# Optimization experiments

Measured on AMD Instinct MI355X. Metric: run time of the kernel, lower is better.

Reference implementation:

```python
import jax, jax.numpy as jnp
import numpy as np

STRIDE = (16, 16)
PADDING = (0, 0)


def setup_inputs() -> dict:
    key = jax.random.key(0)
    k1, k2, k3 = jax.random.split(key, 3)
    x = jax.random.normal(k1, (16, 12, 512, 512), dtype=jnp.float32)
    weight = jax.random.normal(k2, (768, 1, 16, 16), dtype=jnp.float32) * 0.02
    bias = jax.random.normal(k3, (768,), dtype=jnp.float32) * 0.02
    return {"x": x, "weight": weight, "bias": bias}


def reference(x, weight, bias):
    # Faithful to the torch module: groups=c conv with the shared filter
    # repeated per input channel, then mean over the channel axis, then bias.
    b, c, h, w = x.shape
    o = weight.shape[0]
    # groups=c conv with repeated weight == independent conv of each channel
    # with the same (o,1,kh,kw) filter; fold channels into batch.
    xc = x.reshape(b * c, 1, h, w)
    y = jax.lax.conv_general_dilated(
        xc, weight,
        window_strides=STRIDE,
        padding=[(PADDING[0], PADDING[0]), (PADDING[1], PADDING[1])],
        dimension_numbers=("NCHW", "OIHW", "NCHW"),
    )  # (b*c, o, H', W')
    hp, wp = y.shape[-2], y.shape[-1]
    y = y.reshape(b, c, o, hp, wp).mean(axis=1)  # (b, o, H', W')
    y = y + bias[None, :, None, None]
    return y
```

## Files before the change

### kernel.cpp

```cpp
#include <hip/hip_runtime.h>
#include <hip/hip_bf16.h>

#define BATCH 16
#define CIN   12
#define HIMG  512
#define WIMG  512
#define OCH   768
#define KDIM  256
#define HW    (HIMG*WIMG)
#define NPATCH 1024

typedef __attribute__((ext_vector_type(8))) short short8;
typedef __attribute__((ext_vector_type(4))) float f32x4;

__global__ void wpack_kernel(const float* __restrict__ w, short8* __restrict__ wbp) {
    int u = blockIdx.x * 256 + threadIdx.x;
    int lane = u & 63;
    int kk   = (u >> 6) & 7;
    int ot   = u >> 9;
    int o = ot * 16 + (lane & 15);
    int k = kk * 32 + (lane >> 4) * 8;
    const float* src = w + (size_t)o * KDIM + k;
    float4 v0 = *reinterpret_cast<const float4*>(src);
    float4 v1 = *reinterpret_cast<const float4*>(src + 4);
    union { short8 s; __hip_bfloat16 h[8]; } t;
    t.h[0] = __float2bfloat16(v0.x);
    t.h[1] = __float2bfloat16(v0.y);
    t.h[2] = __float2bfloat16(v0.z);
    t.h[3] = __float2bfloat16(v0.w);
    t.h[4] = __float2bfloat16(v1.x);
    t.h[5] = __float2bfloat16(v1.y);
    t.h[6] = __float2bfloat16(v1.z);
    t.h[7] = __float2bfloat16(v1.w);
    wbp[u] = t.s;
}

#define LDB 264

__global__ __launch_bounds__(512, 4) void fused_kernel(
        const short8* __restrict__ wbp,
        const float*  __restrict__ x,
        const float*  __restrict__ bias,
        float* __restrict__ out) {
    __shared__ short Bl[32][LDB];

    const int tid = threadIdx.x;
    const int b  = blockIdx.x >> 5;
    const int is = blockIdx.x & 31;

    {
        const int col = (tid & 127) * 4;
        const int r0  = tid >> 7;
        const int j   = col >> 4;
        const int s0  = col & 15;
        const float* xb = x + (size_t)b * CIN * HW + (size_t)(is * 16) * WIMG + col;
        const float inv = 1.0f / 12.0f;
        #pragma unroll
        for (int p = 0; p < 4; ++p) {
            const int r = p * 4 + r0;
            const float* px = xb + (size_t)r * WIMG;
            float sx = 0.f, sy = 0.f, sz = 0.f, sw = 0.f;
            #pragma unroll
            for (int c = 0; c < CIN; ++c) {
                float4 v = *reinterpret_cast<const float4*>(px + (size_t)c * HW);
                sx += v.x; sy += v.y; sz += v.z; sw += v.w;
            }
            union { ushort4 u4; __hip_bfloat16 h[4]; } o;
            o.h[0] = __float2bfloat16(sx * inv);
            o.h[1] = __float2bfloat16(sy * inv);
            o.h[2] = __float2bfloat16(sz * inv);
            o.h[3] = __float2bfloat16(sw * inv);
            *reinterpret_cast<ushort4*>(&Bl[j][r * 16 + s0]) = o.u4;
        }
    }
    __syncthreads();

    const int lane = tid & 63;
    const int wv   = tid >> 6;
    const int lrow = lane & 15;
    const int lg   = lane >> 4;

    f32x4 acc[6][2] = {};
    const short8* wp = wbp + (size_t)(wv * 6) * 8 * 64 + lane;

    #pragma unroll
    for (int kk = 0; kk < 8; ++kk) {
        short8 af[6], bf[2];
        #pragma unroll
        for (int fo = 0; fo < 6; ++fo)
            af[fo] = wp[(size_t)(fo * 8 + kk) * 64];
        #pragma unroll
        for (int fm = 0; fm < 2; ++fm)
            bf[fm] = *reinterpret_cast<const short8*>(&Bl[fm * 16 + lrow][kk * 32 + lg * 8]);
        #pragma unroll
        for (int fo = 0; fo < 6; ++fo)
            #pragma unroll
            for (int fm = 0; fm < 2; ++fm)
                acc[fo][fm] = __builtin_amdgcn_mfma_f32_16x16x32_bf16(af[fo], bf[fm], acc[fo][fm], 0, 0, 0);
    }

    const int p0 = is * 32;
    float* ob = out + (size_t)b * OCH * NPATCH + p0;
    #pragma unroll
    for (int fo = 0; fo < 6; ++fo) {
        const int obase = wv * 96 + fo * 16 + lg * 4;
        #pragma unroll
        for (int r = 0; r < 4; ++r) {
            const int o = obase + r;
            const float bv = bias[o];
            float* orow = ob + (size_t)o * NPATCH;
            #pragma unroll
            for (int fm = 0; fm < 2; ++fm)
                orow[fm * 16 + lrow] = acc[fo][fm][r] + bv;
        }
    }
}

extern "C" void kernel_launch(void* const* d_in, const int* in_sizes, int n_in,
                              void* d_out, int out_size, void* d_ws, size_t ws_size,
                              hipStream_t stream) {
    const float* x    = (const float*)d_in[0];
    const float* w    = (const float*)d_in[1];
    const float* bias = (const float*)d_in[2];
    float* out = (float*)d_out;

    short8* wbp = (short8*)d_ws;

    wpack_kernel<<<96, 256, 0, stream>>>(w, wbp);
    fused_kernel<<<BATCH * 32, 512, 0, stream>>>(wbp, x, bias, out);
}
```

Measured before the change: 53.51 us.

## Software-pipeline channel-mean loads with MFMA chunks using double buffers

Splits the patch-row reduction into four chunks with two register buffers, so the global loads for the next chunk are issued while the MFMAs consume the finished chunk's K range from LDS. Loads become nontemporal, and the occupancy hint in launch_bounds is removed. The goal is to hide the memory latency of the 12-channel x reads behind compute. The cost is 96 extra VGPRs of buffers and the lost occupancy hint, which can reduce waves per CU. The kernel is mostly bandwidth bound, so the overlap may matter less than occupancy.

```diff
diff --git a/kernel.cpp b/kernel.cpp
--- a/kernel.cpp
+++ b/kernel.cpp
@@ -21,8 +21,8 @@
     int o = ot * 16 + (lane & 15);
     int k = kk * 32 + (lane >> 4) * 8;
     const float* src = w + (size_t)o * KDIM + k;
-    float4 v0 = *reinterpret_cast<const float4*>(src);
-    float4 v1 = *reinterpret_cast<const float4*>(src + 4);
+    f32x4 v0 = *reinterpret_cast<const f32x4*>(src);
+    f32x4 v1 = *reinterpret_cast<const f32x4*>(src + 4);
     union { short8 s; __hip_bfloat16 h[8]; } t;
     t.h[0] = __float2bfloat16(v0.x);
     t.h[1] = __float2bfloat16(v0.y);
@@ -37,7 +37,7 @@
 
 #define LDB 264
 
-__global__ __launch_bounds__(512, 4) void fused_kernel(
+__global__ __launch_bounds__(512) void fused_kernel(
         const short8* __restrict__ wbp,
         const float*  __restrict__ x,
         const float*  __restrict__ bias,
@@ -48,56 +48,84 @@
     const int b  = blockIdx.x >> 5;
     const int is = blockIdx.x & 31;
 
-    {
-        const int col = (tid & 127) * 4;
-        const int r0  = tid >> 7;
-        const int j   = col >> 4;
-        const int s0  = col & 15;
-        const float* xb = x + (size_t)b * CIN * HW + (size_t)(is * 16) * WIMG + col;
-        const float inv = 1.0f / 12.0f;
-        #pragma unroll
-        for (int p = 0; p < 4; ++p) {
-            const int r = p * 4 + r0;
-            const float* px = xb + (size_t)r * WIMG;
-            float sx = 0.f, sy = 0.f, sz = 0.f, sw = 0.f;
-            #pragma unroll
-            for (int c = 0; c < CIN; ++c) {
-                float4 v = *reinterpret_cast<const float4*>(px + (size_t)c * HW);
-                sx += v.x; sy += v.y; sz += v.z; sw += v.w;
-            }
-            union { ushort4 u4; __hip_bfloat16 h[4]; } o;
-            o.h[0] = __float2bfloat16(sx * inv);
-            o.h[1] = __float2bfloat16(sy * inv);
-            o.h[2] = __float2bfloat16(sz * inv);
-            o.h[3] = __float2bfloat16(sw * inv);
-            *reinterpret_cast<ushort4*>(&Bl[j][r * 16 + s0]) = o.u4;
-        }
-    }
-    __syncthreads();
+    const int col = (tid & 127) * 4;
+    const int r0  = tid >> 7;
+    const int j   = col >> 4;
+    const int s0  = col & 15;
+    const float* xb = x + (size_t)b * CIN * HW + (size_t)(is * 16) * WIMG + col;
+    const float inv = 1.0f / 12.0f;
 
     const int lane = tid & 63;
     const int wv   = tid >> 6;
     const int lrow = lane & 15;
     const int lg   = lane >> 4;
+    const short8* wp = wbp + (size_t)(wv * 6) * 8 * 64 + lane;
 
     f32x4 acc[6][2] = {};
-    const short8* wp = wbp + (size_t)(wv * 6) * 8 * 64 + lane;
+    f32x4 bufA[CIN], bufB[CIN];
 
-    #pragma unroll
-    for (int kk = 0; kk < 8; ++kk) {
-        short8 af[6], bf[2];
-        #pragma unroll
-        for (int fo = 0; fo < 6; ++fo)
-            af[fo] = wp[(size_t)(fo * 8 + kk) * 64];
-        #pragma unroll
-        for (int fm = 0; fm < 2; ++fm)
-            bf[fm] = *reinterpret_cast<const short8*>(&Bl[fm * 16 + lrow][kk * 32 + lg * 8]);
-        #pragma unroll
-        for (int fo = 0; fo < 6; ++fo)
-            #pragma unroll
-            for (int fm = 0; fm < 2; ++fm)
-                acc[fo][fm] = __builtin_amdgcn_mfma_f32_16x16x32_bf16(af[fo], bf[fm], acc[fo][fm], 0, 0, 0);
+#define ISSUE(buf, ch)                                                         \
+    {                                                                          \
+        const float* p_ = xb + (size_t)((ch) * 4 + r0) * WIMG;                 \
+        _Pragma("unroll")                                                      \
+        for (int c = 0; c < CIN; ++c)                                          \
+            buf[c] = __builtin_nontemporal_load(                               \
+                reinterpret_cast<const f32x4*>(p_ + (size_t)c * HW));          \
     }
+
+#define REDUCE_STORE(buf, ch)                                                  \
+    {                                                                          \
+        float sx = 0.f, sy = 0.f, sz = 0.f, sw = 0.f;                          \
+        _Pragma("unroll")                                                      \
+        for (int c = 0; c < CIN; ++c) {                                        \
+            sx += buf[c].x; sy += buf[c].y; sz += buf[c].z; sw += buf[c].w;    \
+        }                                                                      \
+        union { ushort4 u4; __hip_bfloat16 h[4]; } o_;                         \
+        o_.h[0] = __float2bfloat16(sx * inv);                                  \
+        o_.h[1] = __float2bfloat16(sy * inv);                                  \
+        o_.h[2] = __float2bfloat16(sz * inv);                                  \
+        o_.h[3] = __float2bfloat16(sw * inv);                                  \
+        *reinterpret_cast<ushort4*>(&Bl[j][((ch) * 4 + r0) * 16 + s0]) = o_.u4;\
+    }
+
+#define MFMA_CHUNK(ch)                                                         \
+    {                                                                          \
+        _Pragma("unroll")                                                      \
+        for (int k2 = 0; k2 < 2; ++k2) {                                       \
+            const int kk = (ch) * 2 + k2;                                      \
+            short8 af[6], bf[2];                                               \
+            _Pragma("unroll")                                                  \
+            for (int fo = 0; fo < 6; ++fo)                                     \
+                af[fo] = wp[(size_t)(fo * 8 + kk) * 64];                       \
+            _Pragma("unroll")                                                  \
+            for (int fm = 0; fm < 2; ++fm)                                     \
+                bf[fm] = *reinterpret_cast<const short8*>(                     \
+                    &Bl[fm * 16 + lrow][kk * 32 + lg * 8]);                    \
+            _Pragma("unroll")                                                  \
+            for (int fo = 0; fo < 6; ++fo)                                     \
+                _Pragma("unroll")                                              \
+                for (int fm = 0; fm < 2; ++fm)                                 \
+                    acc[fo][fm] = __builtin_amdgcn_mfma_f32_16x16x32_bf16(     \
+                        af[fo], bf[fm], acc[fo][fm], 0, 0, 0);                 \
+        }                                                                      \
+    }
+
+    ISSUE(bufA, 0);
+    ISSUE(bufB, 1);
+    REDUCE_STORE(bufA, 0);
+    __syncthreads();
+    ISSUE(bufA, 2);
+    MFMA_CHUNK(0);
+    REDUCE_STORE(bufB, 1);
+    __syncthreads();
+    ISSUE(bufB, 3);
+    MFMA_CHUNK(1);
+    REDUCE_STORE(bufA, 2);
+    __syncthreads();
+    MFMA_CHUNK(2);
+    REDUCE_STORE(bufB, 3);
+    __syncthreads();
+    MFMA_CHUNK(3);
 
     const int p0 = is * 32;
     float* ob = out + (size_t)b * OCH * NPATCH + p0;
```

Measured after the change: 59.09 us. 10.4% more time.

## Split channel-mean into a wide standalone kernel merged with weight packing

Applied to the files above, without the earlier changes.

Moves the 12-channel mean reduction out of the 512-block GEMM kernel into a separate 4096-block kernel that writes a bf16 mean image to workspace. The weight-pack work is folded into the same launch as extra blocks. The GEMM kernel now loads the precomputed bf16 tile. The aim is to raise memory-level parallelism for the dominant input read, at the cost of an extra intermediate write and read and a kernel boundary.

```diff
diff --git a/kernel.cpp b/kernel.cpp
--- a/kernel.cpp
+++ b/kernel.cpp
@@ -10,37 +10,63 @@
 #define HW    (HIMG*WIMG)
 #define NPATCH 1024
 
+#define MEAN_BLOCKS 4096
+#define PACK_BLOCKS 96
+
 typedef __attribute__((ext_vector_type(8))) short short8;
 typedef __attribute__((ext_vector_type(4))) float f32x4;
 
-__global__ void wpack_kernel(const float* __restrict__ w, short8* __restrict__ wbp) {
-    int u = blockIdx.x * 256 + threadIdx.x;
-    int lane = u & 63;
-    int kk   = (u >> 6) & 7;
-    int ot   = u >> 9;
-    int o = ot * 16 + (lane & 15);
-    int k = kk * 32 + (lane >> 4) * 8;
-    const float* src = w + (size_t)o * KDIM + k;
-    float4 v0 = *reinterpret_cast<const float4*>(src);
-    float4 v1 = *reinterpret_cast<const float4*>(src + 4);
-    union { short8 s; __hip_bfloat16 h[8]; } t;
-    t.h[0] = __float2bfloat16(v0.x);
-    t.h[1] = __float2bfloat16(v0.y);
-    t.h[2] = __float2bfloat16(v0.z);
-    t.h[3] = __float2bfloat16(v0.w);
-    t.h[4] = __float2bfloat16(v1.x);
-    t.h[5] = __float2bfloat16(v1.y);
-    t.h[6] = __float2bfloat16(v1.z);
-    t.h[7] = __float2bfloat16(v1.w);
-    wbp[u] = t.s;
+__global__ __launch_bounds__(256) void mean_pack_kernel(
+        const float* __restrict__ x, __hip_bfloat16* __restrict__ xm,
+        const float* __restrict__ w, short8* __restrict__ wbp) {
+    const int bid = blockIdx.x;
+    if (bid < MEAN_BLOCKS) {
+        int idx = bid * 256 + threadIdx.x;
+        int b = idx >> 16;
+        int pos = (idx & 65535) << 2;
+        const float* px = x + (size_t)b * CIN * HW + pos;
+        float sx = 0.f, sy = 0.f, sz = 0.f, sw = 0.f;
+        #pragma unroll
+        for (int c = 0; c < CIN; ++c) {
+            f32x4 v = *reinterpret_cast<const f32x4*>(px + (size_t)c * HW);
+            sx += v.x; sy += v.y; sz += v.z; sw += v.w;
+        }
+        const float inv = 1.0f / 12.0f;
+        union { ushort4 u4; __hip_bfloat16 h[4]; } o;
+        o.h[0] = __float2bfloat16(sx * inv);
+        o.h[1] = __float2bfloat16(sy * inv);
+        o.h[2] = __float2bfloat16(sz * inv);
+        o.h[3] = __float2bfloat16(sw * inv);
+        *reinterpret_cast<ushort4*>(xm + (size_t)idx * 4) = o.u4;
+    } else {
+        int u = (bid - MEAN_BLOCKS) * 256 + threadIdx.x;
+        int lane = u & 63;
+        int kk   = (u >> 6) & 7;
+        int ot   = u >> 9;
+        int o = ot * 16 + (lane & 15);
+        int k = kk * 32 + (lane >> 4) * 8;
+        const float* src = w + (size_t)o * KDIM + k;
+        f32x4 v0 = *reinterpret_cast<const f32x4*>(src);
+        f32x4 v1 = *reinterpret_cast<const f32x4*>(src + 4);
+        union { short8 s; __hip_bfloat16 h[8]; } t;
+        t.h[0] = __float2bfloat16(v0.x);
+        t.h[1] = __float2bfloat16(v0.y);
+        t.h[2] = __float2bfloat16(v0.z);
+        t.h[3] = __float2bfloat16(v0.w);
+        t.h[4] = __float2bfloat16(v1.x);
+        t.h[5] = __float2bfloat16(v1.y);
+        t.h[6] = __float2bfloat16(v1.z);
+        t.h[7] = __float2bfloat16(v1.w);
+        wbp[u] = t.s;
+    }
 }
 
 #define LDB 264
 
-__global__ __launch_bounds__(512, 4) void fused_kernel(
+__global__ __launch_bounds__(512, 4) void gemm_kernel(
         const short8* __restrict__ wbp,
-        const float*  __restrict__ x,
-        const float*  __restrict__ bias,
+        const __hip_bfloat16* __restrict__ xm,
+        const float* __restrict__ bias,
         float* __restrict__ out) {
     __shared__ short Bl[32][LDB];
 
@@ -49,29 +75,12 @@
     const int is = blockIdx.x & 31;
 
     {
-        const int col = (tid & 127) * 4;
-        const int r0  = tid >> 7;
-        const int j   = col >> 4;
-        const int s0  = col & 15;
-        const float* xb = x + (size_t)b * CIN * HW + (size_t)(is * 16) * WIMG + col;
-        const float inv = 1.0f / 12.0f;
-        #pragma unroll
-        for (int p = 0; p < 4; ++p) {
-            const int r = p * 4 + r0;
-            const float* px = xb + (size_t)r * WIMG;
-            float sx = 0.f, sy = 0.f, sz = 0.f, sw = 0.f;
-            #pragma unroll
-            for (int c = 0; c < CIN; ++c) {
-                float4 v = *reinterpret_cast<const float4*>(px + (size_t)c * HW);
-                sx += v.x; sy += v.y; sz += v.z; sw += v.w;
-            }
-            union { ushort4 u4; __hip_bfloat16 h[4]; } o;
-            o.h[0] = __float2bfloat16(sx * inv);
-            o.h[1] = __float2bfloat16(sy * inv);
-            o.h[2] = __float2bfloat16(sz * inv);
-            o.h[3] = __float2bfloat16(sw * inv);
-            *reinterpret_cast<ushort4*>(&Bl[j][r * 16 + s0]) = o.u4;
-        }
+        const int r = tid >> 5;
+        const int j = tid & 31;
+        const short* src = reinterpret_cast<const short*>(
+            xm + (size_t)b * HW + (size_t)(is * 16 + r) * WIMG + j * 16);
+        *reinterpret_cast<short8*>(&Bl[j][r * 16])     = *reinterpret_cast<const short8*>(src);
+        *reinterpret_cast<short8*>(&Bl[j][r * 16 + 8]) = *reinterpret_cast<const short8*>(src + 8);
     }
     __syncthreads();
 
@@ -124,8 +133,9 @@
     const float* bias = (const float*)d_in[2];
     float* out = (float*)d_out;
 
-    short8* wbp = (short8*)d_ws;
+    __hip_bfloat16* xm = (__hip_bfloat16*)d_ws;
+    short8* wbp = (short8*)((char*)d_ws + (size_t)BATCH * HW * 2);
 
-    wpack_kernel<<<96, 256, 0, stream>>>(w, wbp);
-    fused_kernel<<<BATCH * 32, 512, 0, stream>>>(wbp, x, bias, out);
+    mean_pack_kernel<<<MEAN_BLOCKS + PACK_BLOCKS, 256, 0, stream>>>(x, xm, w, wbp);
+    gemm_kernel<<<BATCH * 32, 512, 0, stream>>>(wbp, xm, bias, out);
 }
```

Measured after the change: 54.23 us. Within noise of the previous version (+1.4%).
